# Kernel optimization log

Hardware: AMD Instinct MI355X
Metric: run time of the kernel (lower is better)

Reference implementation:

```python
import jax, jax.numpy as jnp
import numpy as np

EPS = 1e-5
DIL = 1
PAD = 1
STRIDE = 1

def conv2d(x, w, stride=1, pad=1, dil=1):
    return jax.lax.conv_general_dilated(x, w, (stride, stride), [(pad, pad), (pad, pad)],
                                        rhs_dilation=(dil, dil),
                                        dimension_numbers=('NCHW', 'OIHW', 'NCHW'))

def batchnorm(x, g, b, m, v):
    inv = g / jnp.sqrt(v + EPS)
    return x * inv[None, :, None, None] + (b - m * inv)[None, :, None, None]

def _bilinear(img, y, x):
    # img: [C,H,W]; y,x: [Ho,Wo] float sample coords; zero padding outside.
    H, W = img.shape[1], img.shape[2]
    y0 = jnp.floor(y); x0 = jnp.floor(x)
    ty = y - y0; tx = x - x0
    y0i = y0.astype(jnp.int32); x0i = x0.astype(jnp.int32)
    def g(yi, xi):
        valid = (yi >= 0) & (yi < H) & (xi >= 0) & (xi < W)
        v = img[:, jnp.clip(yi, 0, H - 1), jnp.clip(xi, 0, W - 1)]  # [C,Ho,Wo]
        return jnp.where(valid[None], v, jnp.zeros((), img.dtype))
    return (g(y0i, x0i) * ((1 - ty) * (1 - tx))[None]
            + g(y0i, x0i + 1) * ((1 - ty) * tx)[None]
            + g(y0i + 1, x0i) * (ty * (1 - tx))[None]
            + g(y0i + 1, x0i + 1) * (ty * tx)[None])

def deform_conv(x, w, offset, stride=1, pad=1, dil=1):
    # offset: [B, 18, Ho, Wo], channels 0:9 = dy per kernel tap (row-major), 9:18 = dx.
    B, C, H, W = x.shape
    Co = w.shape[0]
    Ho = (H + 2 * pad - dil * 2 - 1) // stride + 1
    Wo = (W + 2 * pad - dil * 2 - 1) // stride + 1
    off = offset.reshape(B, 2, 9, Ho, Wo)
    iy = (jnp.arange(Ho) * stride - pad).astype(x.dtype)
    ix = (jnp.arange(Wo) * stride - pad).astype(x.dtype)
    wk = w.reshape(Co, C, 9)
    out = jnp.zeros((B, Co, Ho, Wo), x.dtype)
    for k in range(9):  # fixed 3x3 kernel taps
        ky, kx = k // 3, k % 3
        ys = iy[:, None] + ky * dil + off[:, 0, k]  # [B,Ho,Wo]
        xs = ix[None, :] + kx * dil + off[:, 1, k]
        val = jax.vmap(_bilinear)(x, ys, xs)        # [B,C,Ho,Wo]
        out = out + jnp.einsum('bchw,oc->bohw', val, wk[:, :, k])
    return out

def offset_bias(dil, dtype):
    bw = jnp.array([[-1., 0., 1.]] * 3, dtype) * (dil - 1)
    bh = bw.T
    return jnp.concatenate([bh.reshape(-1), bw.reshape(-1)])  # [18]

def setup_inputs() -> dict:
    key = jax.random.key(0)
    ks = jax.random.split(key, 12)
    B, C, H, W = 8, 256, 56, 56
    inp = {
        'x': jax.random.normal(ks[0], (B, C, H, W), jnp.float32),
        'conv1_w': jax.random.normal(ks[1], (C, C, 3, 3), jnp.float32) * 0.02,
        'bn1_g': jax.random.normal(ks[2], (C,), jnp.float32) * 0.1 + 1.0,
        'bn1_b': jax.random.normal(ks[3], (C,), jnp.float32) * 0.1,
        'bn1_m': jax.random.normal(ks[4], (C,), jnp.float32) * 0.1,
        'bn1_v': jax.random.uniform(ks[5], (C,), jnp.float32) + 0.5,
        'off_w': jax.random.normal(ks[6], (18, C, 3, 3), jnp.float32) * 0.01,
        'off_b': jnp.zeros((18,), jnp.float32),
        'conv2_w': jax.random.normal(ks[7], (C, C, 3, 3), jnp.float32) * 0.02,
        'bn2_g': jax.random.normal(ks[8], (C,), jnp.float32) * 0.1 + 1.0,
        'bn2_b': jax.random.normal(ks[9], (C,), jnp.float32) * 0.1,
        'bn2_m': jax.random.normal(ks[10], (C,), jnp.float32) * 0.1,
        'bn2_v': jax.random.uniform(ks[11], (C,), jnp.float32) + 0.5,
    }
    return inp

def reference(x, conv1_w, bn1_g, bn1_b, bn1_m, bn1_v, off_w, off_b, conv2_w, bn2_g, bn2_b, bn2_m, bn2_v):
    residual = x
    out = conv2d(x, conv1_w, STRIDE, PAD, DIL)
    out = jax.nn.relu(batchnorm(out, bn1_g, bn1_b, bn1_m, bn1_v))
    offset = conv2d(out, off_w, STRIDE, PAD, DIL) + off_b[None, :, None, None]
    offset = offset + offset_bias(DIL, out.dtype)[None, :, None, None]
    out = deform_conv(out, conv2_w, offset, STRIDE, PAD, DIL)
    out = batchnorm(out, bn2_g, bn2_b, bn2_m, bn2_v)
    return jax.nn.relu(out + residual)
```

## Files before the change

### kernel.cpp

```cpp
#include <hip/hip_runtime.h>

#define NB 8
#define NH 56
#define NW 56
#define NHW 3136
#define NCHW 802816
#define NPIX 25088
#define NHP 58
#define EPSV 1e-5f
#define BUFS 20480

typedef float f32x4 __attribute__((ext_vector_type(4)));
typedef __bf16 bf16x8 __attribute__((ext_vector_type(8)));

__device__ __forceinline__ unsigned short f2b(float f) {
  unsigned int u = __float_as_uint(f);
  u += 0x7FFFu + ((u >> 16) & 1u);
  return (unsigned short)(u >> 16);
}
__device__ __forceinline__ float blo(unsigned int u){ return __uint_as_float(u << 16); }
__device__ __forceinline__ float bhi(unsigned int u){ return __uint_as_float(u & 0xFFFF0000u); }
__device__ __forceinline__ unsigned int pack_trunc(float f0, float f1) {
  return __builtin_amdgcn_perm(__float_as_uint(f1), __float_as_uint(f0), 0x07060302u);
}
__device__ __forceinline__ void soft_barrier() {
  __builtin_amdgcn_s_waitcnt(0xC07F);
  __builtin_amdgcn_s_barrier();
}

__global__ __launch_bounds__(256) void clear_borders(
    unsigned short* __restrict__ xbp, unsigned short* __restrict__ t1b)
{
  int i = blockIdx.x*256 + threadIdx.x;
  int q = i & 31; int pid = i >> 5;
  int b = pid / 228, j = pid % 228;
  int y, x;
  if (j < 58)       { y = 0;  x = j; }
  else if (j < 116) { y = 57; x = j - 58; }
  else { int jj = j - 116; y = 1 + (jj >> 1); x = (jj & 1) * 57; }
  size_t addr = ((size_t)(b*NHP + y)*NHP + x)*256 + q*8;
  uint4 z = make_uint4(0u,0u,0u,0u);
  *(uint4*)(xbp + addr) = z;
  *(uint4*)(t1b + addr) = z;
}

__global__ __launch_bounds__(256) void prep_x(
    const float* __restrict__ x, unsigned short* __restrict__ xbp)
{
  __shared__ float T[64][65];
  const int pxt  = blockIdx.x * 64;
  const int cg   = blockIdx.y * 64;
  const int b    = pxt / NHW;
  const int rem0 = pxt % NHW;
  const int t    = threadIdx.x;
  const int pl   = t & 63;
  const int c0   = t >> 6;
  const float* src = x + (size_t)b*NCHW + rem0;
  #pragma unroll
  for (int it = 0; it < 16; ++it) {
    int c = c0 + it*4;
    T[c][pl] = src[(size_t)(cg + c)*NHW + pl];
  }
  __syncthreads();
  const int pr = t >> 5;
  const int cp = t & 31;
  #pragma unroll
  for (int it = 0; it < 8; ++it) {
    int pxl = pr + it*8;
    int rem = rem0 + pxl;
    int ho = rem / NW, wo = rem % NW;
    unsigned int pk = ((unsigned int)f2b(T[cp*2+1][pxl]) << 16) | (unsigned int)f2b(T[cp*2][pxl]);
    *(unsigned int*)(xbp + ((size_t)(b*NHP + ho + 1)*NHP + (wo + 1))*256 + cg + cp*2) = pk;
  }
}

__global__ __launch_bounds__(256) void prep_w(
    const float* __restrict__ w, unsigned short* __restrict__ wp)
{
  int i = blockIdx.x*256 + threadIdx.x;
  int co = i / 2304;
  int r  = i % 2304;
  int k  = r >> 8;
  int ci = r & 255;
  wp[i] = f2b(w[((size_t)co*256 + ci)*9 + k]);
}

__global__ __launch_bounds__(256) void prep_w3(
    const float* __restrict__ ow, unsigned short* __restrict__ w3p)
{
  int i = blockIdx.x*256 + threadIdx.x;
  int co = i / 2304;
  int r  = i % 2304;
  int k  = r >> 8;
  int ci = r & 255;
  w3p[i] = (co < 18) ? f2b(ow[((size_t)co*256 + ci)*9 + k]) : (unsigned short)0;
}

__global__ __launch_bounds__(512, 4) void gemm_conv1(
    const unsigned short* __restrict__ xbp, const unsigned short* __restrict__ w1p,
    const float* __restrict__ gam, const float* __restrict__ bet,
    const float* __restrict__ mu,  const float* __restrict__ var,
    unsigned short* __restrict__ t1b)
{
  __shared__ unsigned short SMEM[2*BUFS];

  const int bx   = blockIdx.x;
  const int nbx  = (bx & 7)*49 + (bx >> 3);
  const int m0   = nbx * 64;
  const int t    = threadIdx.x;
  const int lane = t & 63;
  const int wv   = t >> 6;
  const int wvM  = wv & 1;
  const int wvN  = wv >> 1;
  const int quad = lane >> 4;
  const int l15  = lane & 15;

  const int srow = t >> 3;
  const int seg  = t & 7;
  const int sxor = srow & 7;
  const int px  = m0 + srow;
  const int b   = px / NHW, rem = px % NHW;
  const int ho  = rem / NW, wo = rem % NW;
  const unsigned int pbase = ((unsigned int)(b*NHP + ho)*NHP + wo)*256u + seg*8u;

  f32x4 acc[2][4];
  #pragma unroll
  for (int i = 0; i < 2; ++i)
    #pragma unroll
    for (int j = 0; j < 4; ++j) acc[i][j] = (f32x4)(0.f);

  uint4 pA, pB0, pB1, pB2, pB3;
  {
    pA  = *(const uint4*)(xbp + pbase);
    const unsigned int rb = seg*8u;
    pB0 = *(const uint4*)(w1p + (size_t)(srow      )*2304 + rb);
    pB1 = *(const uint4*)(w1p + (size_t)(srow +  64)*2304 + rb);
    pB2 = *(const uint4*)(w1p + (size_t)(srow + 128)*2304 + rb);
    pB3 = *(const uint4*)(w1p + (size_t)(srow + 192)*2304 + rb);
    *(uint4*)(&SMEM[srow*64 + ((seg ^ sxor)*8)]) = pA;
    *(uint4*)(&SMEM[4096 + (srow      )*64 + ((seg ^ sxor)*8)]) = pB0;
    *(uint4*)(&SMEM[4096 + (srow +  64)*64 + ((seg ^ sxor)*8)]) = pB1;
    *(uint4*)(&SMEM[4096 + (srow + 128)*64 + ((seg ^ sxor)*8)]) = pB2;
    *(uint4*)(&SMEM[4096 + (srow + 192)*64 + ((seg ^ sxor)*8)]) = pB3;
    pA  = *(const uint4*)(xbp + pbase + 64u);
    const unsigned int rb1 = 64u + seg*8u;
    pB0 = *(const uint4*)(w1p + (size_t)(srow      )*2304 + rb1);
    pB1 = *(const uint4*)(w1p + (size_t)(srow +  64)*2304 + rb1);
    pB2 = *(const uint4*)(w1p + (size_t)(srow + 128)*2304 + rb1);
    pB3 = *(const uint4*)(w1p + (size_t)(srow + 192)*2304 + rb1);
    soft_barrier();
  }

  for (int r = 0; r < 36; ++r) {
    unsigned short* Ac = SMEM + (r & 1)*BUFS;
    unsigned short* Bc = Ac + 4096;
    unsigned short* An = SMEM + ((r + 1) & 1)*BUFS;
    unsigned short* Bn = An + 4096;
    *(uint4*)(&An[srow*64 + ((seg ^ sxor)*8)]) = pA;
    *(uint4*)(&Bn[(srow      )*64 + ((seg ^ sxor)*8)]) = pB0;
    *(uint4*)(&Bn[(srow +  64)*64 + ((seg ^ sxor)*8)]) = pB1;
    *(uint4*)(&Bn[(srow + 128)*64 + ((seg ^ sxor)*8)]) = pB2;
    *(uint4*)(&Bn[(srow + 192)*64 + ((seg ^ sxor)*8)]) = pB3;
    {
      const int rn = (r < 34) ? r + 2 : 35;
      const int kn = rn >> 2, cicn = rn & 3;
      const int kyn = kn/3, kxn = kn - kyn*3;
      pA  = *(const uint4*)(xbp + pbase + (unsigned int)((kyn*NHP + kxn)*256 + cicn*64));
      const unsigned int rb = (unsigned int)(rn*64) + seg*8u;
      pB0 = *(const uint4*)(w1p + (size_t)(srow      )*2304 + rb);
      pB1 = *(const uint4*)(w1p + (size_t)(srow +  64)*2304 + rb);
      pB2 = *(const uint4*)(w1p + (size_t)(srow + 128)*2304 + rb);
      pB3 = *(const uint4*)(w1p + (size_t)(srow + 192)*2304 + rb);
    }
    #pragma unroll
    for (int kk = 0; kk < 2; ++kk) {
      const int s8 = (kk*4 + quad) ^ (l15 & 7);
      bf16x8 af[2], bfr[4];
      #pragma unroll
      for (int mt = 0; mt < 2; ++mt)
        af[mt] = *(const bf16x8*)(&Ac[(wvM*32 + mt*16 + l15)*64 + s8*8]);
      #pragma unroll
      for (int nt = 0; nt < 4; ++nt)
        bfr[nt] = *(const bf16x8*)(&Bc[(wvN*64 + nt*16 + l15)*64 + s8*8]);
      #pragma unroll
      for (int mt = 0; mt < 2; ++mt)
        #pragma unroll
        for (int nt = 0; nt < 4; ++nt)
          acc[mt][nt] = __builtin_amdgcn_mfma_f32_16x16x32_bf16(af[mt], bfr[nt], acc[mt][nt], 0, 0, 0);
    }
    soft_barrier();
  }

  __syncthreads();
  unsigned short* Sw = SMEM + wv*2304;
  #pragma unroll
  for (int nt = 0; nt < 4; ++nt) {
    const int co = wvN*64 + nt*16 + l15;
    const float inv  = gam[co] * rsqrtf(var[co] + EPSV);
    const float beta = bet[co] - mu[co]*inv;
    #pragma unroll
    for (int mt = 0; mt < 2; ++mt) {
      #pragma unroll
      for (int rr = 0; rr < 4; ++rr) {
        const int pxl = mt*16 + quad*4 + rr;
        float val = acc[mt][nt][rr]*inv + beta;
        val = val > 0.f ? val : 0.f;
        Sw[pxl*72 + nt*16 + l15] = f2b(val);
      }
    }
  }
  #pragma unroll
  for (int i = 0; i < 4; ++i) {
    const int pxl = (lane >> 3) + 8*i;
    const int sc  = lane & 7;
    uint4 q = *(const uint4*)(&Sw[pxl*72 + sc*8]);
    const int pg = m0 + wvM*32 + pxl;
    const int bb = pg / NHW, rm = pg % NHW;
    const int hh = rm / NW, ww = rm % NW;
    *(uint4*)(t1b + ((size_t)(bb*NHP + hh + 1)*NHP + ww + 1)*256 + wvN*64 + sc*8) = q;
  }
}

__global__ __launch_bounds__(256, 8) void gemm_off(
    const unsigned short* __restrict__ t1b, const unsigned short* __restrict__ w3p,
    const float* __restrict__ ob, float* __restrict__ toff)
{
  __shared__ unsigned short Al[4096];
  __shared__ unsigned short Bl[2048];

  const int bx  = blockIdx.x;
  const int nbx = (bx & 7)*49 + (bx >> 3);
  const int m0  = nbx * 64;
  const int kc = blockIdx.y;
  const int t    = threadIdx.x;
  const int lane = t & 63;
  const int wv   = t >> 6;
  const int quad = lane >> 4;
  const int l15  = lane & 15;

  const int arow = t >> 2;
  const int as4  = t & 3;
  const int axor = arow & 7;
  const int pxa  = m0 + arow;
  const int ba   = pxa / NHW, rema = pxa % NHW;
  const unsigned int pbase = ((unsigned int)(ba*NHP + rema/NW)*NHP + rema%NW)*256u;

  const int brow = t >> 3;
  const int bs   = t & 7;

  f32x4 acc[2];
  #pragma unroll
  for (int nt = 0; nt < 2; ++nt) {
    float init = 0.f;
    if (kc == 0) { int co = nt*16 + l15; init = (co < 18) ? ob[co] : 0.f; }
    acc[nt] = (f32x4)(init);
  }

  uint4 pA0, pA1, pB;
  {
    const int r = kc*9, k = r >> 2, cic = r & 3;
    const int ky = k/3, kx = k - ky*3;
    const unsigned int base = pbase + (unsigned int)((ky*NHP + kx)*256 + cic*64);
    pA0 = *(const uint4*)(t1b + base + as4*8);
    pA1 = *(const uint4*)(t1b + base + (as4+4)*8);
    pB  = *(const uint4*)(w3p + (size_t)brow*2304 + r*64 + bs*8);
  }

  for (int rr = 0; rr < 9; ++rr) {
    const int r = kc*9 + rr;
    __syncthreads();
    *(uint4*)(&Al[arow*64 + ((as4     ^ axor)*8)]) = pA0;
    *(uint4*)(&Al[arow*64 + (((as4+4) ^ axor)*8)]) = pA1;
    *(uint4*)(&Bl[brow*64 + ((bs ^ (brow & 7))*8)]) = pB;
    {
      const int rn = (rr < 8) ? r + 1 : r;
      const int kn = rn >> 2, cicn = rn & 3;
      const int kyn = kn/3, kxn = kn - kyn*3;
      const unsigned int base = pbase + (unsigned int)((kyn*NHP + kxn)*256 + cicn*64);
      pA0 = *(const uint4*)(t1b + base + as4*8);
      pA1 = *(const uint4*)(t1b + base + (as4+4)*8);
      pB  = *(const uint4*)(w3p + (size_t)brow*2304 + rn*64 + bs*8);
    }
    soft_barrier();
    #pragma unroll
    for (int kk = 0; kk < 2; ++kk) {
      const int s8 = (kk*4 + quad) ^ (l15 & 7);
      bf16x8 af = *(const bf16x8*)(&Al[(wv*16 + l15)*64 + s8*8]);
      #pragma unroll
      for (int nt = 0; nt < 2; ++nt) {
        bf16x8 bfr = *(const bf16x8*)(&Bl[(nt*16 + l15)*64 + s8*8]);
        acc[nt] = __builtin_amdgcn_mfma_f32_16x16x32_bf16(af, bfr, acc[nt], 0, 0, 0);
      }
    }
  }
  #pragma unroll
  for (int nt = 0; nt < 2; ++nt) {
    const int co = nt*16 + l15;
    if (co < 18) {
      #pragma unroll
      for (int rr2 = 0; rr2 < 4; ++rr2) {
        const int pg = m0 + wv*16 + quad*4 + rr2;
        const int bb = pg / NHW, rm = pg % NHW;
        atomicAdd(&toff[(size_t)bb*(18*NHW) + (size_t)co*NHW + rm], acc[nt][rr2]);
      }
    }
  }
}

__global__ __launch_bounds__(512, 4) void gemm_deform(
    const unsigned short* __restrict__ t1b, const unsigned short* __restrict__ w2p,
    const float* __restrict__ toff, const float* __restrict__ xres,
    const float* __restrict__ gam, const float* __restrict__ bet,
    const float* __restrict__ mu,  const float* __restrict__ var,
    float* __restrict__ outp)
{
  __shared__ unsigned short SMEM[2*BUFS];

  const int bid  = blockIdx.x;
  const int nb   = (bid & 7)*49 + (bid >> 3);
  const int m0   = nb * 64;
  const int t    = threadIdx.x;
  const int lane = t & 63;
  const int wv   = t >> 6;
  const int wvM  = wv & 1;
  const int wvN  = wv >> 1;
  const int quad = lane >> 4;
  const int l15  = lane & 15;

  const int srow = t >> 3;
  const int seg  = t & 7;
  const int sxor = srow & 7;
  const int px   = m0 + srow;
  const int b    = px / NHW, rem = px % NHW;
  const int ho   = rem / NW, wo = rem % NW;
  const int obb  = b*(18*NHW) + rem;
  const unsigned int prowb = (unsigned int)(b*NHP);

  f32x4 acc[2][4];
  #pragma unroll
  for (int i = 0; i < 2; ++i)
    #pragma unroll
    for (int j = 0; j < 4; ++j) acc[i][j] = (f32x4)(0.f);

  unsigned int o00, o01, o10, o11;
  float w00, w01, w10, w11;
#define COORDS(KK) {                                                   \
    const int ky_ = (KK)/3, kx_ = (KK) - ky_*3;                        \
    const float offy = toff[obb + (KK)*NHW];                           \
    const float offx = toff[obb + (9+(KK))*NHW];                       \
    const float yf = (float)(ho - 1 + ky_) + offy;                     \
    const float xf = (float)(wo - 1 + kx_) + offx;                     \
    const float y0f = floorf(yf), x0f = floorf(xf);                    \
    const float ty = yf - y0f,   tx = xf - x0f;                        \
    const int y0p = (int)y0f + 1, x0p = (int)x0f + 1;                  \
    const int cy0 = min(max(y0p,   0), NHP-1);                         \
    const int cy1 = min(max(y0p+1, 0), NHP-1);                         \
    const int cx0 = min(max(x0p,   0), NHP-1);                         \
    const int cx1 = min(max(x0p+1, 0), NHP-1);                         \
    w00 = (1.f-ty)*(1.f-tx);  w01 = (1.f-ty)*tx;                       \
    w10 = ty*(1.f-tx);        w11 = ty*tx;                             \
    o00 = ((prowb + cy0)*NHP + cx0)*256u + seg*8u;                     \
    o01 = ((prowb + cy0)*NHP + cx1)*256u + seg*8u;                     \
    o10 = ((prowb + cy1)*NHP + cx0)*256u + seg*8u;                     \
    o11 = ((prowb + cy1)*NHP + cx1)*256u + seg*8u;                     \
  }

#define PACK_WRITE(DST) {                                                        \
    uint4 res;                                                                   \
    { float a0 = w00*blo(pc00.x) + w01*blo(pc01.x) + w10*blo(pc10.x) + w11*blo(pc11.x); \
      float a1 = w00*bhi(pc00.x) + w01*bhi(pc01.x) + w10*bhi(pc10.x) + w11*bhi(pc11.x); \
      res.x = pack_trunc(a0, a1); }                                              \
    { float a0 = w00*blo(pc00.y) + w01*blo(pc01.y) + w10*blo(pc10.y) + w11*blo(pc11.y); \
      float a1 = w00*bhi(pc00.y) + w01*bhi(pc01.y) + w10*bhi(pc10.y) + w11*bhi(pc11.y); \
      res.y = pack_trunc(a0, a1); }                                              \
    { float a0 = w00*blo(pc00.z) + w01*blo(pc01.z) + w10*blo(pc10.z) + w11*blo(pc11.z); \
      float a1 = w00*bhi(pc00.z) + w01*bhi(pc01.z) + w10*bhi(pc10.z) + w11*bhi(pc11.z); \
      res.z = pack_trunc(a0, a1); }                                              \
    { float a0 = w00*blo(pc00.w) + w01*blo(pc01.w) + w10*blo(pc10.w) + w11*blo(pc11.w); \
      float a1 = w00*bhi(pc00.w) + w01*bhi(pc01.w) + w10*bhi(pc10.w) + w11*bhi(pc11.w); \
      res.w = pack_trunc(a0, a1); }                                              \
    *(uint4*)(&(DST)[srow*64 + ((seg ^ sxor)*8)]) = res;                         \
  }

  COORDS(0);
  uint4 pc00, pc01, pc10, pc11, pB0, pB1, pB2, pB3;
  {
    pc00 = *(const uint4*)(t1b + o00);
    pc01 = *(const uint4*)(t1b + o01);
    pc10 = *(const uint4*)(t1b + o10);
    pc11 = *(const uint4*)(t1b + o11);
    const unsigned int rb = seg*8u;
    pB0 = *(const uint4*)(w2p + (size_t)(srow      )*2304 + rb);
    pB1 = *(const uint4*)(w2p + (size_t)(srow +  64)*2304 + rb);
    pB2 = *(const uint4*)(w2p + (size_t)(srow + 128)*2304 + rb);
    pB3 = *(const uint4*)(w2p + (size_t)(srow + 192)*2304 + rb);
    PACK_WRITE(SMEM);
    *(uint4*)(&SMEM[4096 + (srow      )*64 + ((seg ^ sxor)*8)]) = pB0;
    *(uint4*)(&SMEM[4096 + (srow +  64)*64 + ((seg ^ sxor)*8)]) = pB1;
    *(uint4*)(&SMEM[4096 + (srow + 128)*64 + ((seg ^ sxor)*8)]) = pB2;
    *(uint4*)(&SMEM[4096 + (srow + 192)*64 + ((seg ^ sxor)*8)]) = pB3;
    pc00 = *(const uint4*)(t1b + o00 + 64u);
    pc01 = *(const uint4*)(t1b + o01 + 64u);
    pc10 = *(const uint4*)(t1b + o10 + 64u);
    pc11 = *(const uint4*)(t1b + o11 + 64u);
    const unsigned int rb1 = 64u + seg*8u;
    pB0 = *(const uint4*)(w2p + (size_t)(srow      )*2304 + rb1);
    pB1 = *(const uint4*)(w2p + (size_t)(srow +  64)*2304 + rb1);
    pB2 = *(const uint4*)(w2p + (size_t)(srow + 128)*2304 + rb1);
    pB3 = *(const uint4*)(w2p + (size_t)(srow + 192)*2304 + rb1);
    soft_barrier();
  }

  for (int r = 0; r < 36; ++r) {
    unsigned short* Ac = SMEM + (r & 1)*BUFS;
    unsigned short* Bc = Ac + 4096;
    unsigned short* An = SMEM + ((r + 1) & 1)*BUFS;
    unsigned short* Bn = An + 4096;
    PACK_WRITE(An);
    *(uint4*)(&Bn[(srow      )*64 + ((seg ^ sxor)*8)]) = pB0;
    *(uint4*)(&Bn[(srow +  64)*64 + ((seg ^ sxor)*8)]) = pB1;
    *(uint4*)(&Bn[(srow + 128)*64 + ((seg ^ sxor)*8)]) = pB2;
    *(uint4*)(&Bn[(srow + 192)*64 + ((seg ^ sxor)*8)]) = pB3;
    if ((r & 3) == 2 && r < 34) COORDS((r + 2) >> 2);
    {
      const int rn = (r < 34) ? r + 2 : 35;
      const unsigned int cio = (unsigned int)((rn & 3)*64);
      pc00 = *(const uint4*)(t1b + o00 + cio);
      pc01 = *(const uint4*)(t1b + o01 + cio);
      pc10 = *(const uint4*)(t1b + o10 + cio);
      pc11 = *(const uint4*)(t1b + o11 + cio);
      const unsigned int rb = (unsigned int)(rn*64) + seg*8u;
      pB0 = *(const uint4*)(w2p + (size_t)(srow      )*2304 + rb);
      pB1 = *(const uint4*)(w2p + (size_t)(srow +  64)*2304 + rb);
      pB2 = *(const uint4*)(w2p + (size_t)(srow + 128)*2304 + rb);
      pB3 = *(const uint4*)(w2p + (size_t)(srow + 192)*2304 + rb);
    }
    #pragma unroll
    for (int kk = 0; kk < 2; ++kk) {
      const int s8 = (kk*4 + quad) ^ (l15 & 7);
      bf16x8 af[2], bfr[4];
      #pragma unroll
      for (int mt = 0; mt < 2; ++mt)
        af[mt] = *(const bf16x8*)(&Ac[(wvM*32 + mt*16 + l15)*64 + s8*8]);
      #pragma unroll
      for (int nt = 0; nt < 4; ++nt)
        bfr[nt] = *(const bf16x8*)(&Bc[(wvN*64 + nt*16 + l15)*64 + s8*8]);
      #pragma unroll
      for (int mt = 0; mt < 2; ++mt)
        #pragma unroll
        for (int nt = 0; nt < 4; ++nt)
          acc[mt][nt] = __builtin_amdgcn_mfma_f32_16x16x32_bf16(af[mt], bfr[nt], acc[mt][nt], 0, 0, 0);
    }
    soft_barrier();
  }
#undef COORDS
#undef PACK_WRITE

  __syncthreads();
  float* Sl = (float*)SMEM + wv*1056;
  const int pxl_r = lane & 31;
  const int csel  = lane >> 5;
  const int pg    = m0 + wvM*32 + pxl_r;
  const int bo    = pg / NHW, remo = pg % NHW;
  const size_t obase = (size_t)bo*NCHW + remo;
  #pragma unroll
  for (int h = 0; h < 2; ++h) {
    #pragma unroll
    for (int nt2 = 0; nt2 < 2; ++nt2) {
      const int nt = h*2 + nt2;
      #pragma unroll
      for (int mt = 0; mt < 2; ++mt) {
        #pragma unroll
        for (int rr = 0; rr < 4; ++rr) {
          const int pxl = mt*16 + quad*4 + rr;
          Sl[pxl*33 + nt2*16 + l15] = acc[mt][nt][rr];
        }
      }
    }
    #pragma unroll
    for (int j = 0; j < 16; ++j) {
      const int col = csel*16 + j;
      const int co  = wvN*64 + h*32 + col;
      const float inv  = gam[co] * rsqrtf(var[co] + EPSV);
      const float beta = bet[co] - mu[co]*inv;
      const size_t off = obase + (size_t)co*NHW;
      float val = Sl[pxl_r*33 + col];
      float o = val*inv + beta + xres[off];
      outp[off] = o > 0.f ? o : 0.f;
    }
  }
}

extern "C" void kernel_launch(void* const* d_in, const int* in_sizes, int n_in,
                              void* d_out, int out_size, void* d_ws, size_t ws_size,
                              hipStream_t stream) {
  const float* x   = (const float*)d_in[0];
  const float* w1  = (const float*)d_in[1];
  const float* g1  = (const float*)d_in[2];
  const float* b1  = (const float*)d_in[3];
  const float* m1  = (const float*)d_in[4];
  const float* v1  = (const float*)d_in[5];
  const float* ow  = (const float*)d_in[6];
  const float* ob  = (const float*)d_in[7];
  const float* w2  = (const float*)d_in[8];
  const float* g2  = (const float*)d_in[9];
  const float* b2  = (const float*)d_in[10];
  const float* m2  = (const float*)d_in[11];
  const float* v2  = (const float*)d_in[12];
  float* out = (float*)d_out;

  const size_t PADSZ = (size_t)NB*NHP*NHP*256;
  unsigned short* xbp = (unsigned short*)d_ws;
  unsigned short* t1b = xbp + PADSZ;
  float*          tof = (float*)(t1b + PADSZ);
  unsigned short* w1p = (unsigned short*)(tof + (size_t)NB*18*NHW);
  unsigned short* w2p = w1p + (size_t)589824;
  unsigned short* w3p = w2p + (size_t)589824;

  clear_borders<<<228, 256, 0, stream>>>(xbp, t1b);
  dim3 gp(392, 4, 1);
  prep_x<<<gp, 256, 0, stream>>>(x, xbp);
  prep_w<<<2304, 256, 0, stream>>>(w1, w1p);
  prep_w<<<2304, 256, 0, stream>>>(w2, w2p);
  prep_w3<<<288, 256, 0, stream>>>(ow, w3p);
  hipMemsetAsync(tof, 0, (size_t)NB*18*NHW*sizeof(float), stream);

  gemm_conv1<<<392, 512, 0, stream>>>(xbp, w1p, g1, b1, m1, v1, t1b);
  dim3 go(392, 4, 1);
  gemm_off<<<go, 256, 0, stream>>>(t1b, w3p, ob, tof);
  gemm_deform<<<392, 512, 0, stream>>>(t1b, w2p, tof, x, g2, b2, m2, v2, out);
}
```

Before: 250.7 us.

## Double threads per GEMM block and merge setup kernels

The conv1 and deform GEMM kernels now run 1024 threads (16 waves) per block instead of 512. Each wave owns a 16x64 output tile rather than 32x64, and the per-thread global-load and bilinear gather work is halved. The three weight-prep kernels are merged into a single launch, and the offset-buffer memset is folded into the border-clear kernel to cut launch overhead. The trade-off is that each wave reuses its B fragments across half as many MFMAs, giving more LDS reads per MFMA, and barriers now synchronise more waves.

```diff
diff --git a/kernel.cpp b/kernel.cpp
--- a/kernel.cpp
+++ b/kernel.cpp
@@ -9,6 +9,7 @@
 #define NHP 58
 #define EPSV 1e-5f
 #define BUFS 20480
+#define TOFN 451584
 
 typedef float f32x4 __attribute__((ext_vector_type(4)));
 typedef __bf16 bf16x8 __attribute__((ext_vector_type(8)));
@@ -29,7 +30,8 @@
 }
 
 __global__ __launch_bounds__(256) void clear_borders(
-    unsigned short* __restrict__ xbp, unsigned short* __restrict__ t1b)
+    unsigned short* __restrict__ xbp, unsigned short* __restrict__ t1b,
+    float* __restrict__ tof)
 {
   int i = blockIdx.x*256 + threadIdx.x;
   int q = i & 31; int pid = i >> 5;
@@ -42,6 +44,11 @@
   uint4 z = make_uint4(0u,0u,0u,0u);
   *(uint4*)(xbp + addr) = z;
   *(uint4*)(t1b + addr) = z;
+  int zi = i*8;
+  if (zi < TOFN) {
+    *(float4*)(tof + zi)     = make_float4(0.f,0.f,0.f,0.f);
+    *(float4*)(tof + zi + 4) = make_float4(0.f,0.f,0.f,0.f);
+  }
 }
 
 __global__ __launch_bounds__(256) void prep_x(
@@ -74,29 +81,28 @@
   }
 }
 
-__global__ __launch_bounds__(256) void prep_w(
-    const float* __restrict__ w, unsigned short* __restrict__ wp)
+__global__ __launch_bounds__(256) void prep_w_all(
+    const float* __restrict__ w1, const float* __restrict__ w2,
+    const float* __restrict__ ow,
+    unsigned short* __restrict__ w1p, unsigned short* __restrict__ w2p,
+    unsigned short* __restrict__ w3p)
 {
   int i = blockIdx.x*256 + threadIdx.x;
-  int co = i / 2304;
-  int r  = i % 2304;
-  int k  = r >> 8;
-  int ci = r & 255;
-  wp[i] = f2b(w[((size_t)co*256 + ci)*9 + k]);
-}
-
-__global__ __launch_bounds__(256) void prep_w3(
-    const float* __restrict__ ow, unsigned short* __restrict__ w3p)
-{
-  int i = blockIdx.x*256 + threadIdx.x;
-  int co = i / 2304;
-  int r  = i % 2304;
-  int k  = r >> 8;
-  int ci = r & 255;
-  w3p[i] = (co < 18) ? f2b(ow[((size_t)co*256 + ci)*9 + k]) : (unsigned short)0;
-}
-
-__global__ __launch_bounds__(512, 4) void gemm_conv1(
+  if (i < 589824) {
+    int co = i / 2304, r = i % 2304, k = r >> 8, ci = r & 255;
+    w1p[i] = f2b(w1[((size_t)co*256 + ci)*9 + k]);
+  } else if (i < 1179648) {
+    int j = i - 589824;
+    int co = j / 2304, r = j % 2304, k = r >> 8, ci = r & 255;
+    w2p[j] = f2b(w2[((size_t)co*256 + ci)*9 + k]);
+  } else {
+    int j = i - 1179648;
+    int co = j / 2304, r = j % 2304, k = r >> 8, ci = r & 255;
+    w3p[j] = (co < 18) ? f2b(ow[((size_t)co*256 + ci)*9 + k]) : (unsigned short)0;
+  }
+}
+
+__global__ __launch_bounds__(1024, 4) void gemm_conv1(
     const unsigned short* __restrict__ xbp, const unsigned short* __restrict__ w1p,
     const float* __restrict__ gam, const float* __restrict__ bet,
     const float* __restrict__ mu,  const float* __restrict__ var,
@@ -110,44 +116,40 @@
   const int t    = threadIdx.x;
   const int lane = t & 63;
   const int wv   = t >> 6;
-  const int wvM  = wv & 1;
-  const int wvN  = wv >> 1;
+  const int wvM  = wv & 3;
+  const int wvN  = wv >> 2;
   const int quad = lane >> 4;
   const int l15  = lane & 15;
 
-  const int srow = t >> 3;
-  const int seg  = t & 7;
-  const int sxor = srow & 7;
-  const int px  = m0 + srow;
+  const int srowA = t >> 4;
+  const int seg15 = t & 15;
+  const int aoff  = srowA*64 + (((seg15 >> 1) ^ (srowA & 7))*8 + (seg15 & 1)*4);
+  const int rowB  = t >> 2;
+  const int bs2   = (t & 3)*2;
+  const int boff0 = rowB*64 + (((bs2    ) ^ (rowB & 7))*8);
+  const int boff1 = rowB*64 + (((bs2 + 1) ^ (rowB & 7))*8);
+
+  const int px  = m0 + srowA;
   const int b   = px / NHW, rem = px % NHW;
   const int ho  = rem / NW, wo = rem % NW;
-  const unsigned int pbase = ((unsigned int)(b*NHP + ho)*NHP + wo)*256u + seg*8u;
-
-  f32x4 acc[2][4];
-  #pragma unroll
-  for (int i = 0; i < 2; ++i)
-    #pragma unroll
-    for (int j = 0; j < 4; ++j) acc[i][j] = (f32x4)(0.f);
-
-  uint4 pA, pB0, pB1, pB2, pB3;
+  const unsigned int pbase = ((unsigned int)(b*NHP + ho)*NHP + wo)*256u + seg15*4u;
+
+  f32x4 acc[4];
+  #pragma unroll
+  for (int j = 0; j < 4; ++j) acc[j] = (f32x4)(0.f);
+
+  uint2 pA;
+  uint4 pB0, pB1;
   {
-    pA  = *(const uint4*)(xbp + pbase);
-    const unsigned int rb = seg*8u;
-    pB0 = *(const uint4*)(w1p + (size_t)(srow      )*2304 + rb);
-    pB1 = *(const uint4*)(w1p + (size_t)(srow +  64)*2304 + rb);
-    pB2 = *(const uint4*)(w1p + (size_t)(srow + 128)*2304 + rb);
-    pB3 = *(const uint4*)(w1p + (size_t)(srow + 192)*2304 + rb);
-    *(uint4*)(&SMEM[srow*64 + ((seg ^ sxor)*8)]) = pA;
-    *(uint4*)(&SMEM[4096 + (srow      )*64 + ((seg ^ sxor)*8)]) = pB0;
-    *(uint4*)(&SMEM[4096 + (srow +  64)*64 + ((seg ^ sxor)*8)]) = pB1;
-    *(uint4*)(&SMEM[4096 + (srow + 128)*64 + ((seg ^ sxor)*8)]) = pB2;
-    *(uint4*)(&SMEM[4096 + (srow + 192)*64 + ((seg ^ sxor)*8)]) = pB3;
-    pA  = *(const uint4*)(xbp + pbase + 64u);
-    const unsigned int rb1 = 64u + seg*8u;
-    pB0 = *(const uint4*)(w1p + (size_t)(srow      )*2304 + rb1);
-    pB1 = *(const uint4*)(w1p + (size_t)(srow +  64)*2304 + rb1);
-    pB2 = *(const uint4*)(w1p + (size_t)(srow + 128)*2304 + rb1);
-    pB3 = *(const uint4*)(w1p + (size_t)(srow + 192)*2304 + rb1);
+    uint2 tA  = *(const uint2*)(xbp + pbase);
+    uint4 tB0 = *(const uint4*)(w1p + (size_t)rowB*2304 + bs2*8);
+    uint4 tB1 = *(const uint4*)(w1p + (size_t)rowB*2304 + bs2*8 + 8);
+    *(uint2*)(&SMEM[aoff]) = tA;
+    *(uint4*)(&SMEM[4096 + boff0]) = tB0;
+    *(uint4*)(&SMEM[4096 + boff1]) = tB1;
+    pA  = *(const uint2*)(xbp + pbase + 64u);
+    pB0 = *(const uint4*)(w1p + (size_t)rowB*2304 + 64 + bs2*8);
+    pB1 = *(const uint4*)(w1p + (size_t)rowB*2304 + 64 + bs2*8 + 8);
     soft_barrier();
   }
 
@@ -156,65 +158,54 @@
     unsigned short* Bc = Ac + 4096;
     unsigned short* An = SMEM + ((r + 1) & 1)*BUFS;
     unsigned short* Bn = An + 4096;
-    *(uint4*)(&An[srow*64 + ((seg ^ sxor)*8)]) = pA;
-    *(uint4*)(&Bn[(srow      )*64 + ((seg ^ sxor)*8)]) = pB0;
-    *(uint4*)(&Bn[(srow +  64)*64 + ((seg ^ sxor)*8)]) = pB1;
-    *(uint4*)(&Bn[(srow + 128)*64 + ((seg ^ sxor)*8)]) = pB2;
-    *(uint4*)(&Bn[(srow + 192)*64 + ((seg ^ sxor)*8)]) = pB3;
+    *(uint2*)(&An[aoff]) = pA;
+    *(uint4*)(&Bn[boff0]) = pB0;
+    *(uint4*)(&Bn[boff1]) = pB1;
     {
       const int rn = (r < 34) ? r + 2 : 35;
       const int kn = rn >> 2, cicn = rn & 3;
       const int kyn = kn/3, kxn = kn - kyn*3;
-      pA  = *(const uint4*)(xbp + pbase + (unsigned int)((kyn*NHP + kxn)*256 + cicn*64));
-      const unsigned int rb = (unsigned int)(rn*64) + seg*8u;
-      pB0 = *(const uint4*)(w1p + (size_t)(srow      )*2304 + rb);
-      pB1 = *(const uint4*)(w1p + (size_t)(srow +  64)*2304 + rb);
-      pB2 = *(const uint4*)(w1p + (size_t)(srow + 128)*2304 + rb);
-      pB3 = *(const uint4*)(w1p + (size_t)(srow + 192)*2304 + rb);
+      pA  = *(const uint2*)(xbp + pbase + (unsigned int)((kyn*NHP + kxn)*256 + cicn*64));
+      const unsigned int rb = (unsigned int)(rn*64) + bs2*8u;
+      pB0 = *(const uint4*)(w1p + (size_t)rowB*2304 + rb);
+      pB1 = *(const uint4*)(w1p + (size_t)rowB*2304 + rb + 8);
     }
     #pragma unroll
     for (int kk = 0; kk < 2; ++kk) {
       const int s8 = (kk*4 + quad) ^ (l15 & 7);
-      bf16x8 af[2], bfr[4];
-      #pragma unroll
-      for (int mt = 0; mt < 2; ++mt)
-        af[mt] = *(const bf16x8*)(&Ac[(wvM*32 + mt*16 + l15)*64 + s8*8]);
+      bf16x8 af = *(const bf16x8*)(&Ac[(wvM*16 + l15)*64 + s8*8]);
+      bf16x8 bfr[4];
       #pragma unroll
       for (int nt = 0; nt < 4; ++nt)
         bfr[nt] = *(const bf16x8*)(&Bc[(wvN*64 + nt*16 + l15)*64 + s8*8]);
       #pragma unroll
-      for (int mt = 0; mt < 2; ++mt)
-        #pragma unroll
-        for (int nt = 0; nt < 4; ++nt)
-          acc[mt][nt] = __builtin_amdgcn_mfma_f32_16x16x32_bf16(af[mt], bfr[nt], acc[mt][nt], 0, 0, 0);
+      for (int nt = 0; nt < 4; ++nt)
+        acc[nt] = __builtin_amdgcn_mfma_f32_16x16x32_bf16(af, bfr[nt], acc[nt], 0, 0, 0);
     }
     soft_barrier();
   }
 
   __syncthreads();
-  unsigned short* Sw = SMEM + wv*2304;
+  unsigned short* Sw = SMEM + wv*1152;
   #pragma unroll
   for (int nt = 0; nt < 4; ++nt) {
     const int co = wvN*64 + nt*16 + l15;
     const float inv  = gam[co] * rsqrtf(var[co] + EPSV);
     const float beta = bet[co] - mu[co]*inv;
     #pragma unroll
-    for (int mt = 0; mt < 2; ++mt) {
-      #pragma unroll
-      for (int rr = 0; rr < 4; ++rr) {
-        const int pxl = mt*16 + quad*4 + rr;
-        float val = acc[mt][nt][rr]*inv + beta;
-        val = val > 0.f ? val : 0.f;
-        Sw[pxl*72 + nt*16 + l15] = f2b(val);
-      }
-    }
-  }
-  #pragma unroll
-  for (int i = 0; i < 4; ++i) {
+    for (int rr = 0; rr < 4; ++rr) {
+      const int pxl = quad*4 + rr;
+      float val = acc[nt][rr]*inv + beta;
+      val = val > 0.f ? val : 0.f;
+      Sw[pxl*72 + nt*16 + l15] = f2b(val);
+    }
+  }
+  #pragma unroll
+  for (int i = 0; i < 2; ++i) {
     const int pxl = (lane >> 3) + 8*i;
     const int sc  = lane & 7;
     uint4 q = *(const uint4*)(&Sw[pxl*72 + sc*8]);
-    const int pg = m0 + wvM*32 + pxl;
+    const int pg = m0 + wvM*16 + pxl;
     const int bb = pg / NHW, rm = pg % NHW;
     const int hh = rm / NW, ww = rm % NW;
     *(uint4*)(t1b + ((size_t)(bb*NHP + hh + 1)*NHP + ww + 1)*256 + wvN*64 + sc*8) = q;
@@ -307,7 +298,7 @@
   }
 }
 
-__global__ __launch_bounds__(512, 4) void gemm_deform(
+__global__ __launch_bounds__(1024, 4) void gemm_deform(
     const unsigned short* __restrict__ t1b, const unsigned short* __restrict__ w2p,
     const float* __restrict__ toff, const float* __restrict__ xres,
     const float* __restrict__ gam, const float* __restrict__ bet,
@@ -322,25 +313,28 @@
   const int t    = threadIdx.x;
   const int lane = t & 63;
   const int wv   = t >> 6;
-  const int wvM  = wv & 1;
-  const int wvN  = wv >> 1;
+  const int wvM  = wv & 3;
+  const int wvN  = wv >> 2;
   const int quad = lane >> 4;
   const int l15  = lane & 15;
 
-  const int srow = t >> 3;
-  const int seg  = t & 7;
-  const int sxor = srow & 7;
-  const int px   = m0 + srow;
+  const int srowA = t >> 4;
+  const int seg15 = t & 15;
+  const int aoff  = srowA*64 + (((seg15 >> 1) ^ (srowA & 7))*8 + (seg15 & 1)*4);
+  const int rowB  = t >> 2;
+  const int bs2   = (t & 3)*2;
+  const int boff0 = rowB*64 + (((bs2    ) ^ (rowB & 7))*8);
+  const int boff1 = rowB*64 + (((bs2 + 1) ^ (rowB & 7))*8);
+
+  const int px   = m0 + srowA;
   const int b    = px / NHW, rem = px % NHW;
   const int ho   = rem / NW, wo = rem % NW;
   const int obb  = b*(18*NHW) + rem;
   const unsigned int prowb = (unsigned int)(b*NHP);
 
-  f32x4 acc[2][4];
-  #pragma unroll
-  for (int i = 0; i < 2; ++i)
-    #pragma unroll
-    for (int j = 0; j < 4; ++j) acc[i][j] = (f32x4)(0.f);
+  f32x4 acc[4];
+  #pragma unroll
+  for (int j = 0; j < 4; ++j) acc[j] = (f32x4)(0.f);
 
   unsigned int o00, o01, o10, o11;
   float w00, w01, w10, w11;
@@ -359,55 +353,48 @@
     const int cx1 = min(max(x0p+1, 0), NHP-1);                         \
     w00 = (1.f-ty)*(1.f-tx);  w01 = (1.f-ty)*tx;                       \
     w10 = ty*(1.f-tx);        w11 = ty*tx;                             \
-    o00 = ((prowb + cy0)*NHP + cx0)*256u + seg*8u;                     \
-    o01 = ((prowb + cy0)*NHP + cx1)*256u + seg*8u;                     \
-    o10 = ((prowb + cy1)*NHP + cx0)*256u + seg*8u;                     \
-    o11 = ((prowb + cy1)*NHP + cx1)*256u + seg*8u;                     \
-  }
-
-#define PACK_WRITE(DST) {                                                        \
-    uint4 res;                                                                   \
+    o00 = ((prowb + cy0)*NHP + cx0)*256u + seg15*4u;                   \
+    o01 = ((prowb + cy0)*NHP + cx1)*256u + seg15*4u;                   \
+    o10 = ((prowb + cy1)*NHP + cx0)*256u + seg15*4u;                   \
+    o11 = ((prowb + cy1)*NHP + cx1)*256u + seg15*4u;                   \
+  }
+
+#define PACKW(DST) {                                                            \
+    uint2 res;                                                                  \
     { float a0 = w00*blo(pc00.x) + w01*blo(pc01.x) + w10*blo(pc10.x) + w11*blo(pc11.x); \
       float a1 = w00*bhi(pc00.x) + w01*bhi(pc01.x) + w10*bhi(pc10.x) + w11*bhi(pc11.x); \
-      res.x = pack_trunc(a0, a1); }                                              \
+      res.x = pack_trunc(a0, a1); }                                             \
     { float a0 = w00*blo(pc00.y) + w01*blo(pc01.y) + w10*blo(pc10.y) + w11*blo(pc11.y); \
       float a1 = w00*bhi(pc00.y) + w01*bhi(pc01.y) + w10*bhi(pc10.y) + w11*bhi(pc11.y); \
-      res.y = pack_trunc(a0, a1); }                                              \
-    { float a0 = w00*blo(pc00.z) + w01*blo(pc01.z) + w10*blo(pc10.z) + w11*blo(pc11.z); \
-      float a1 = w00*bhi(pc00.z) + w01*bhi(pc01.z) + w10*bhi(pc10.z) + w11*bhi(pc11.z); \
-      res.z = pack_trunc(a0, a1); }                                              \
-    { float a0 = w00*blo(pc00.w) + w01*blo(pc01.w) + w10*blo(pc10.w) + w11*blo(pc11.w); \
-      float a1 = w00*bhi(pc00.w) + w01*bhi(pc01.w) + w10*bhi(pc10.w) + w11*bhi(pc11.w); \
-      res.w = pack_trunc(a0, a1); }                                              \
-    *(uint4*)(&(DST)[srow*64 + ((seg ^ sxor)*8)]) = res;                         \
-  }
+      res.y = pack_trunc(a0, a1); }                                             \
+    *(uint2*)(&(DST)[aoff]) = res;                                              \
+  }
+
+#define ISSUEC(RN) {                                                           \
+    const unsigned int cio_ = (unsigned int)(((RN) & 3)*64);                   \
+    pc00 = *(const uint2*)(t1b + o00 + cio_);                                  \
+    pc01 = *(const uint2*)(t1b + o01 + cio_);                                  \
+    pc10 = *(const uint2*)(t1b + o10 + cio_);                                  \
+    pc11 = *(const uint2*)(t1b + o11 + cio_);                                  \
+  }
+#define ISSUEB(RN) {                                                           \
+    const unsigned int rb_ = (unsigned int)((RN)*64) + bs2*8u;                 \
+    pB0 = *(const uint4*)(w2p + (size_t)rowB*2304 + rb_);                      \
+    pB1 = *(const uint4*)(w2p + (size_t)rowB*2304 + rb_ + 8);                  \
+  }
+
+  uint2 pc00, pc01, pc10, pc11;
+  uint4 pB0, pB1;
 
   COORDS(0);
-  uint4 pc00, pc01, pc10, pc11, pB0, pB1, pB2, pB3;
   {
-    pc00 = *(const uint4*)(t1b + o00);
-    pc01 = *(const uint4*)(t1b + o01);
-    pc10 = *(const uint4*)(t1b + o10);
-    pc11 = *(const uint4*)(t1b + o11);
-    const unsigned int rb = seg*8u;
-    pB0 = *(const uint4*)(w2p + (size_t)(srow      )*2304 + rb);
-    pB1 = *(const uint4*)(w2p + (size_t)(srow +  64)*2304 + rb);
-    pB2 = *(const uint4*)(w2p + (size_t)(srow + 128)*2304 + rb);
-    pB3 = *(const uint4*)(w2p + (size_t)(srow + 192)*2304 + rb);
-    PACK_WRITE(SMEM);
-    *(uint4*)(&SMEM[4096 + (srow      )*64 + ((seg ^ sxor)*8)]) = pB0;
-    *(uint4*)(&SMEM[4096 + (srow +  64)*64 + ((seg ^ sxor)*8)]) = pB1;
-    *(uint4*)(&SMEM[4096 + (srow + 128)*64 + ((seg ^ sxor)*8)]) = pB2;
-    *(uint4*)(&SMEM[4096 + (srow + 192)*64 + ((seg ^ sxor)*8)]) = pB3;
-    pc00 = *(const uint4*)(t1b + o00 + 64u);
-    pc01 = *(const uint4*)(t1b + o01 + 64u);
-    pc10 = *(const uint4*)(t1b + o10 + 64u);
-    pc11 = *(const uint4*)(t1b + o11 + 64u);
-    const unsigned int rb1 = 64u + seg*8u;
-    pB0 = *(const uint4*)(w2p + (size_t)(srow      )*2304 + rb1);
-    pB1 = *(const uint4*)(w2p + (size_t)(srow +  64)*2304 + rb1);
-    pB2 = *(const uint4*)(w2p + (size_t)(srow + 128)*2304 + rb1);
-    pB3 = *(const uint4*)(w2p + (size_t)(srow + 192)*2304 + rb1);
+    ISSUEC(0);
+    ISSUEB(0);
+    PACKW(SMEM);
+    *(uint4*)(&SMEM[4096 + boff0]) = pB0;
+    *(uint4*)(&SMEM[4096 + boff1]) = pB1;
+    ISSUEC(1);
+    ISSUEB(1);
     soft_barrier();
   }
 
@@ -416,51 +403,39 @@
     unsigned short* Bc = Ac + 4096;
     unsigned short* An = SMEM + ((r + 1) & 1)*BUFS;
     unsigned short* Bn = An + 4096;
-    PACK_WRITE(An);
-    *(uint4*)(&Bn[(srow      )*64 + ((seg ^ sxor)*8)]) = pB0;
-    *(uint4*)(&Bn[(srow +  64)*64 + ((seg ^ sxor)*8)]) = pB1;
-    *(uint4*)(&Bn[(srow + 128)*64 + ((seg ^ sxor)*8)]) = pB2;
-    *(uint4*)(&Bn[(srow + 192)*64 + ((seg ^ sxor)*8)]) = pB3;
+    PACKW(An);
+    *(uint4*)(&Bn[boff0]) = pB0;
+    *(uint4*)(&Bn[boff1]) = pB1;
     if ((r & 3) == 2 && r < 34) COORDS((r + 2) >> 2);
     {
       const int rn = (r < 34) ? r + 2 : 35;
-      const unsigned int cio = (unsigned int)((rn & 3)*64);
-      pc00 = *(const uint4*)(t1b + o00 + cio);
-      pc01 = *(const uint4*)(t1b + o01 + cio);
-      pc10 = *(const uint4*)(t1b + o10 + cio);
-      pc11 = *(const uint4*)(t1b + o11 + cio);
-      const unsigned int rb = (unsigned int)(rn*64) + seg*8u;
-      pB0 = *(const uint4*)(w2p + (size_t)(srow      )*2304 + rb);
-      pB1 = *(const uint4*)(w2p + (size_t)(srow +  64)*2304 + rb);
-      pB2 = *(const uint4*)(w2p + (size_t)(srow + 128)*2304 + rb);
-      pB3 = *(const uint4*)(w2p + (size_t)(srow + 192)*2304 + rb);
+      ISSUEC(rn);
+      ISSUEB(rn);
     }
     #pragma unroll
     for (int kk = 0; kk < 2; ++kk) {
       const int s8 = (kk*4 + quad) ^ (l15 & 7);
-      bf16x8 af[2], bfr[4];
-      #pragma unroll
-      for (int mt = 0; mt < 2; ++mt)
-        af[mt] = *(const bf16x8*)(&Ac[(wvM*32 + mt*16 + l15)*64 + s8*8]);
+      bf16x8 af = *(const bf16x8*)(&Ac[(wvM*16 + l15)*64 + s8*8]);
+      bf16x8 bfr[4];
       #pragma unroll
       for (int nt = 0; nt < 4; ++nt)
         bfr[nt] = *(const bf16x8*)(&Bc[(wvN*64 + nt*16 + l15)*64 + s8*8]);
       #pragma unroll
-      for (int mt = 0; mt < 2; ++mt)
-        #pragma unroll
-        for (int nt = 0; nt < 4; ++nt)
-          acc[mt][nt] = __builtin_amdgcn_mfma_f32_16x16x32_bf16(af[mt], bfr[nt], acc[mt][nt], 0, 0, 0);
+      for (int nt = 0; nt < 4; ++nt)
+        acc[nt] = __builtin_amdgcn_mfma_f32_16x16x32_bf16(af, bfr[nt], acc[nt], 0, 0, 0);
     }
     soft_barrier();
   }
+#undef ISSUEB
+#undef ISSUEC
+#undef PACKW
 #undef COORDS
-#undef PACK_WRITE
 
   __syncthreads();
-  float* Sl = (float*)SMEM + wv*1056;
-  const int pxl_r = lane & 31;
-  const int csel  = lane >> 5;
-  const int pg    = m0 + wvM*32 + pxl_r;
+  float* Sl = (float*)SMEM + wv*528;
+  const int pxl_r = lane & 15;
+  const int csel  = lane >> 4;
+  const int pg    = m0 + wvM*16 + pxl_r;
   const int bo    = pg / NHW, remo = pg % NHW;
   const size_t obase = (size_t)bo*NCHW + remo;
   #pragma unroll
@@ -469,17 +444,14 @@
     for (int nt2 = 0; nt2 < 2; ++nt2) {
       const int nt = h*2 + nt2;
       #pragma unroll
-      for (int mt = 0; mt < 2; ++mt) {
-        #pragma unroll
-        for (int rr = 0; rr < 4; ++rr) {
-          const int pxl = mt*16 + quad*4 + rr;
-          Sl[pxl*33 + nt2*16 + l15] = acc[mt][nt][rr];
-        }
+      for (int rr = 0; rr < 4; ++rr) {
+        const int pxl = quad*4 + rr;
+        Sl[pxl*33 + nt2*16 + l15] = acc[nt][rr];
       }
     }
     #pragma unroll
-    for (int j = 0; j < 16; ++j) {
-      const int col = csel*16 + j;
+    for (int j = 0; j < 8; ++j) {
+      const int col = csel*8 + j;
       const int co  = wvN*64 + h*32 + col;
       const float inv  = gam[co] * rsqrtf(var[co] + EPSV);
       const float beta = bet[co] - mu[co]*inv;
@@ -517,16 +489,13 @@
   unsigned short* w2p = w1p + (size_t)589824;
   unsigned short* w3p = w2p + (size_t)589824;
 
-  clear_borders<<<228, 256, 0, stream>>>(xbp, t1b);
+  clear_borders<<<228, 256, 0, stream>>>(xbp, t1b, tof);
   dim3 gp(392, 4, 1);
   prep_x<<<gp, 256, 0, stream>>>(x, xbp);
-  prep_w<<<2304, 256, 0, stream>>>(w1, w1p);
-  prep_w<<<2304, 256, 0, stream>>>(w2, w2p);
-  prep_w3<<<288, 256, 0, stream>>>(ow, w3p);
-  hipMemsetAsync(tof, 0, (size_t)NB*18*NHW*sizeof(float), stream);
-
-  gemm_conv1<<<392, 512, 0, stream>>>(xbp, w1p, g1, b1, m1, v1, t1b);
+  prep_w_all<<<4896, 256, 0, stream>>>(w1, w2, ow, w1p, w2p, w3p);
+
+  gemm_conv1<<<392, 1024, 0, stream>>>(xbp, w1p, g1, b1, m1, v1, t1b);
   dim3 go(392, 4, 1);
   gemm_off<<<go, 256, 0, stream>>>(t1b, w3p, ob, tof);
-  gemm_deform<<<392, 512, 0, stream>>>(t1b, w2p, tof, x, g2, b2, m2, v2, out);
-}
+  gemm_deform<<<392, 1024, 0, stream>>>(t1b, w2p, tof, x, g2, b2, m2, v2, out);
+}
```

Result: slower. 273.4 us (+9.1%).
